# Performance work log

Hardware: AMD Instinct MI355X
Metric: run time of the kernel (lower is better)

The kernel has to match this reference:

```python
import jax, jax.numpy as jnp
import numpy as np

ROUTING_ITERS = 3
EPS = 1e-9


def squash(s):
    # s: [..., D]; faithful to the torch code: x / (1 + n^2) / sqrt(n^2 + eps)
    sq = jnp.sum(s * s, axis=-1, keepdims=True)
    return s / (1.0 + sq) / jnp.sqrt(sq + EPS)


def setup_inputs() -> dict:
    key = jax.random.key(0)
    k1, k2 = jax.random.split(key)
    B, I, C, D, d = 64, 4096, 32, 16, 16
    x = jax.random.normal(k1, (B, I, d), dtype=jnp.float32)
    weights = jax.random.normal(k2, (1, I, C, D, d), dtype=jnp.float32)
    return {"x": x, "weights": weights}


def reference(x, weights):
    # u_hat[b,i,c,D] = weights[0,i,c,D,d] @ x[b,i,d]
    u_hat = jnp.einsum('icDd,bid->bicD', weights[0], x)  # [B, I, C, D]
    B, I, C, D = u_hat.shape
    b_ij = jnp.zeros((B, I, C), dtype=u_hat.dtype)
    v_j = None
    for _ in range(ROUTING_ITERS):
        c_ij = jax.nn.softmax(b_ij, axis=2)                     # [B, I, C]
        s_j = jnp.einsum('bic,bicD->bcD', c_ij, u_hat)          # [B, C, D]
        v_j = squash(s_j)                                       # [B, C, D]
        b_ij = b_ij + jnp.einsum('bicD,bcD->bic', u_hat, v_j)   # agreement
    return v_j
```

## Files before the change

### kernel.cpp

```cpp
#include <hip/hip_runtime.h>
#include <math.h>

#define ITILES 256
#define IPB    16

typedef __bf16 bf16x8 __attribute__((ext_vector_type(8)));
typedef float  f32x16 __attribute__((ext_vector_type(16)));

__device__ inline unsigned short f2bf(float f) {
    unsigned int x = __float_as_uint(f);
    x += 0x7fff + ((x >> 16) & 1);
    return (unsigned short)(x >> 16);
}
__device__ inline float bf2f(unsigned short u) {
    return __uint_as_float(((unsigned int)u) << 16);
}
__device__ inline uint4 pack8(const unsigned short* o) {
    uint4 p;
    p.x = o[0] | ((unsigned)o[1] << 16);
    p.y = o[2] | ((unsigned)o[3] << 16);
    p.z = o[4] | ((unsigned)o[5] << 16);
    p.w = o[6] | ((unsigned)o[7] << 16);
    return p;
}

__device__ inline unsigned cvtpk(float lo, float hi) {
    unsigned r;
    asm("v_cvt_pk_bf16_f32 %0, %1, %2" : "=v"(r) : "v"(lo), "v"(hi));
    return r;
}
__device__ inline unsigned split3(float x, float y, unsigned& q2, unsigned& q3) {
    unsigned q1 = cvtpk(x, y);
    float f1x = __uint_as_float(q1 << 16);
    float f1y = __uint_as_float(q1 & 0xffff0000u);
    float rx = x - f1x, ry = y - f1y;
    q2 = cvtpk(rx, ry);
    float f2x = __uint_as_float(q2 << 16);
    float f2y = __uint_as_float(q2 & 0xffff0000u);
    q3 = cvtpk(rx - f2x, ry - f2y);
    return q1;
}

__global__ __launch_bounds__(128) void prep_x(const float* __restrict__ x,
                                              unsigned short* __restrict__ Xp)
{
    const int i = blockIdx.x;
    const int t = threadIdx.x;
    const int b = t >> 1, kh = t & 1;
    const float4* s4 = (const float4*)(x + ((size_t)b * 4096 + i) * 16 + kh * 8);
    float4 wa = s4[0], wb = s4[1];
    float wv[8] = {wa.x, wa.y, wa.z, wa.w, wb.x, wb.y, wb.z, wb.w};
    unsigned short o1[8], o2[8], o3[8];
    #pragma unroll
    for (int j = 0; j < 8; ++j) {
        float w = wv[j];
        o1[j] = f2bf(w);            float f1 = bf2f(o1[j]);
        o2[j] = f2bf(w - f1);       float f2 = bf2f(o2[j]);
        o3[j] = f2bf(w - f1 - f2);
    }
    unsigned short* dst = Xp + (size_t)i * 3072 + kh * 1536 + b * 8;
    *(uint4*)(dst)        = pack8(o1);
    *(uint4*)(dst + 512)  = pack8(o2);
    *(uint4*)(dst + 1024) = pack8(o3);
}

template<int USE_V>
__global__ __launch_bounds__(1024, 4)
void pass_kernel(const float* __restrict__ W,
                 const unsigned short* __restrict__ Xp,
                 const float* __restrict__ vg,
                 float* __restrict__ slab)
{
    __shared__ float4 vt[8192];
    __shared__ float  p_lds[32 * 65];
    __shared__ float  cij_lds[32 * 65];

    const int tid   = threadIdx.x;
    const int mt    = tid >> 6;
    const int lane  = tid & 63;
    const int l31   = lane & 31;
    const int h     = lane >> 5;
    const int cA    = 2 * mt + h;
    const int itile = blockIdx.x;
    const int i0    = itile * IPB;

    const int cW = 2 * mt + ((l31 >> 2) & 1);
    const int DW = (l31 & 3) + 4 * (l31 >> 3);
    const float4* w4 = (const float4*)(W + (size_t)i0 * 8192 + ((cW * 16 + DW) * 16 + h * 8));

    if (USE_V) {
        const float4* v4 = (const float4*)vg;
        #pragma unroll
        for (int k = 0; k < 8; ++k) {
            int idx = k * 1024 + tid;
            int b = idx >> 7, cd = idx & 127;
            vt[b * 128 + (cd ^ (b & 31))] = v4[idx];
        }
        __syncthreads();
    }

    f32x16 s0, s1;
    #pragma unroll
    for (int q = 0; q < 16; ++q) { s0[q] = 0.f; s1[q] = 0.f; }

    float4 wa = w4[0], wb = w4[1];

    #define MF(A_, B_, C_) __builtin_amdgcn_mfma_f32_32x32x16_bf16( \
        __builtin_bit_cast(bf16x8, A_), __builtin_bit_cast(bf16x8, B_), C_, 0, 0, 0)

    for (int ii = 0; ii < IPB; ++ii) {
        const int i = i0 + ii;
        const unsigned short* bb = Xp + (size_t)i * 3072 + (size_t)h * 1536 + l31 * 8;

        uint4 a1, a2, a3;
        a1.x = split3(wa.x, wa.y, a2.x, a3.x);
        a1.y = split3(wa.z, wa.w, a2.y, a3.y);
        a1.z = split3(wb.x, wb.y, a2.z, a3.z);
        a1.w = split3(wb.z, wb.w, a2.w, a3.w);

        {
            const int iin = (ii + 1 < IPB) ? (ii + 1) : ii;
            wa = w4[(size_t)iin * 2048];
            wb = w4[(size_t)iin * 2048 + 1];
        }

        if (USE_V == 0) {
            uint4 b10 = *(const uint4*)(bb);
            uint4 b11 = *(const uint4*)(bb + 256);
            uint4 b20 = *(const uint4*)(bb + 512);
            uint4 b21 = *(const uint4*)(bb + 512 + 256);
            __builtin_amdgcn_s_setprio(1);
            s0 = MF(a1, b10, s0); s1 = MF(a1, b11, s1);
            s0 = MF(a2, b10, s0); s1 = MF(a2, b11, s1);
            __builtin_amdgcn_s_setprio(0);
            uint4 b30 = *(const uint4*)(bb + 1024);
            uint4 b31 = *(const uint4*)(bb + 1024 + 256);
            __builtin_amdgcn_s_setprio(1);
            s0 = MF(a1, b20, s0); s1 = MF(a1, b21, s1);
            s0 = MF(a3, b10, s0); s1 = MF(a3, b11, s1);
            s0 = MF(a2, b20, s0); s1 = MF(a2, b21, s1);
            s0 = MF(a1, b30, s0); s1 = MF(a1, b31, s1);
            __builtin_amdgcn_s_setprio(0);
        } else {
            #pragma unroll
            for (int nt = 0; nt < 2; ++nt) {
                const unsigned short* bp = bb + nt * 256;
                uint4 b1 = *(const uint4*)(bp);
                uint4 b2 = *(const uint4*)(bp + 512);
                uint4 b3 = *(const uint4*)(bp + 1024);

                f32x16 u;
                #pragma unroll
                for (int q = 0; q < 16; ++q) u[q] = 0.f;
                __builtin_amdgcn_s_setprio(1);
                u = MF(a1, b1, u);
                u = MF(a2, b1, u);
                u = MF(a1, b2, u);
                u = MF(a3, b1, u);
                u = MF(a2, b2, u);
                u = MF(a1, b3, u);
                __builtin_amdgcn_s_setprio(0);

                const int b = nt * 32 + l31;
                float p = 0.f;
                #pragma unroll
                for (int dblk = 0; dblk < 4; ++dblk) {
                    float4 vv = vt[b * 128 + ((cA * 4 + dblk) ^ l31)];
                    p = fmaf(u[dblk * 4 + 0], vv.x, p);
                    p = fmaf(u[dblk * 4 + 1], vv.y, p);
                    p = fmaf(u[dblk * 4 + 2], vv.z, p);
                    p = fmaf(u[dblk * 4 + 3], vv.w, p);
                }
                p_lds[cA * 65 + b] = p;
                __syncthreads();

                {
                    const int bsm = nt * 32 + mt * 2 + h;
                    float e = __expf(p_lds[l31 * 65 + bsm]);
                    float t = e;
                    t += __shfl_xor(t, 16); t += __shfl_xor(t, 8);
                    t += __shfl_xor(t, 4);  t += __shfl_xor(t, 2);
                    t += __shfl_xor(t, 1);
                    cij_lds[l31 * 65 + bsm] = __fdividef(e, t);
                }
                __syncthreads();

                {
                    f32x16& ss = nt ? s1 : s0;
                    const float cij = cij_lds[cA * 65 + b];
                    #pragma unroll
                    for (int q = 0; q < 16; ++q) ss[q] = fmaf(cij, u[q], ss[q]);
                }
            }
        }
    }
    #undef MF

    float4* slab4 = (float4*)slab;
    #pragma unroll
    for (int nt = 0; nt < 2; ++nt) {
        const f32x16& ss = nt ? s1 : s0;
        const int b = nt * 32 + l31;
        size_t base = ((size_t)itile * 64 + b) * 128 + cA * 4;
        #pragma unroll
        for (int dblk = 0; dblk < 4; ++dblk) {
            float4 o = {ss[dblk * 4 + 0], ss[dblk * 4 + 1], ss[dblk * 4 + 2], ss[dblk * 4 + 3]};
            slab4[base + dblk] = o;
        }
    }
}

__global__ __launch_bounds__(256)
void reduce_squash(const float* __restrict__ slab, float* __restrict__ out, float scale,
                   const float* __restrict__ v1in, float* __restrict__ vsum)
{
    __shared__ float part[128];
    const int tid  = threadIdx.x;
    const int half = tid >> 7;
    const int o    = blockIdx.x * 128 + (tid & 127);
    float a[8];
    #pragma unroll
    for (int k = 0; k < 8; ++k) a[k] = 0.f;
    for (int g = 0; g < 16; ++g) {
        #pragma unroll
        for (int k = 0; k < 8; ++k)
            a[k] += slab[(size_t)(half * 128 + g * 8 + k) * 32768 + o];
    }
    float s = 0.f;
    #pragma unroll
    for (int k = 0; k < 8; ++k) s += a[k];
    if (half) part[tid & 127] = s;
    __syncthreads();
    if (!half) {
        s = (s + part[tid]) * scale;
        float t = s * s;
        t += __shfl_xor(t, 1);
        t += __shfl_xor(t, 2);
        t += __shfl_xor(t, 4);
        t += __shfl_xor(t, 8);
        float r = s / (1.0f + t) / sqrtf(t + 1e-9f);
        out[o] = r;
        if (v1in) vsum[o] = r + v1in[o];
    }
}

extern "C" void kernel_launch(void* const* d_in, const int* in_sizes, int n_in,
                              void* d_out, int out_size, void* d_ws, size_t ws_size,
                              hipStream_t stream)
{
    const float* x = (const float*)d_in[0];
    const float* W = (const float*)d_in[1];

    float* slab = (float*)d_ws;
    float* v1   = slab + (size_t)ITILES * 32768;
    float* v2   = v1 + 32768;
    float* v12  = v2 + 32768;
    unsigned short* Xp = (unsigned short*)(v12 + 32768);
    float* out  = (float*)d_out;

    hipLaunchKernelGGL(prep_x, dim3(4096), dim3(128), 0, stream, x, Xp);

    hipLaunchKernelGGL((pass_kernel<0>), dim3(ITILES), dim3(1024), 0, stream, W, Xp, (const float*)nullptr, slab);
    hipLaunchKernelGGL(reduce_squash,    dim3(256),    dim3(256),  0, stream, slab, v1, 1.0f / 32.0f, (const float*)nullptr, (float*)nullptr);
    hipLaunchKernelGGL((pass_kernel<1>), dim3(ITILES), dim3(1024), 0, stream, W, Xp, v1, slab);
    hipLaunchKernelGGL(reduce_squash,    dim3(256),    dim3(256),  0, stream, slab, v2, 1.0f, v1, v12);
    hipLaunchKernelGGL((pass_kernel<1>), dim3(ITILES), dim3(1024), 0, stream, W, Xp, v12, slab);
    hipLaunchKernelGGL(reduce_squash,    dim3(256),    dim3(256),  0, stream, slab, out, 1.0f, (const float*)nullptr, (float*)nullptr);
}
```

Before: 364.9 us.

## Split first routing pass into small blocks, deepen W prefetch, widen reduction grid

The first routing pass no longer needs the shared v table or barriers, so it moves to its own kernel with 256-thread blocks (four blocks per i-tile) for better scheduling and occupancy. The later passes prefetch weights two iterations ahead instead of one. The slab reduction now spreads over 1024 blocks of 32 outputs with 8 partial sums each, to use more CUs. The costs are more launched blocks and more register pressure from the deeper prefetch.

Result: slower. 375.8 us (+3.0%).

```diff
diff --git a/kernel.cpp b/kernel.cpp
--- a/kernel.cpp
+++ b/kernel.cpp
@@ -64,12 +64,85 @@
     *(uint4*)(dst + 1024) = pack8(o3);
 }
 
-template<int USE_V>
+#define MF(A_, B_, C_) __builtin_amdgcn_mfma_f32_32x32x16_bf16( \
+    __builtin_bit_cast(bf16x8, A_), __builtin_bit_cast(bf16x8, B_), C_, 0, 0, 0)
+
+__global__ __launch_bounds__(256, 5)
+void pass0_kernel(const float* __restrict__ W,
+                  const unsigned short* __restrict__ Xp,
+                  float* __restrict__ slab)
+{
+    const int tid   = threadIdx.x;
+    const int lane  = tid & 63;
+    const int l31   = lane & 31;
+    const int h     = lane >> 5;
+    const int bid   = blockIdx.x;
+    const int itile = bid >> 2;
+    const int mt    = ((bid & 3) << 2) + (tid >> 6);
+    const int cA    = 2 * mt + h;
+    const int i0    = itile * IPB;
+
+    const int cW = 2 * mt + ((l31 >> 2) & 1);
+    const int DW = (l31 & 3) + 4 * (l31 >> 3);
+    const float4* w4 = (const float4*)(W + (size_t)i0 * 8192 + ((cW * 16 + DW) * 16 + h * 8));
+
+    f32x16 s0, s1;
+    #pragma unroll
+    for (int q = 0; q < 16; ++q) { s0[q] = 0.f; s1[q] = 0.f; }
+
+    float4 wa = w4[0], wb = w4[1];
+
+    for (int ii = 0; ii < IPB; ++ii) {
+        const int i = i0 + ii;
+        const unsigned short* bb = Xp + (size_t)i * 3072 + (size_t)h * 1536 + l31 * 8;
+
+        uint4 a1, a2, a3;
+        a1.x = split3(wa.x, wa.y, a2.x, a3.x);
+        a1.y = split3(wa.z, wa.w, a2.y, a3.y);
+        a1.z = split3(wb.x, wb.y, a2.z, a3.z);
+        a1.w = split3(wb.z, wb.w, a2.w, a3.w);
+
+        {
+            const int iin = (ii + 1 < IPB) ? (ii + 1) : ii;
+            wa = w4[(size_t)iin * 2048];
+            wb = w4[(size_t)iin * 2048 + 1];
+        }
+
+        #pragma unroll
+        for (int nt = 0; nt < 2; ++nt) {
+            const unsigned short* bp = bb + nt * 256;
+            f32x16& ss = nt ? s1 : s0;
+            uint4 b1 = *(const uint4*)(bp);
+            uint4 b2 = *(const uint4*)(bp + 512);
+            ss = MF(a1, b1, ss);
+            ss = MF(a2, b1, ss);
+            uint4 b3 = *(const uint4*)(bp + 1024);
+            ss = MF(a1, b2, ss);
+            ss = MF(a3, b1, ss);
+            ss = MF(a2, b2, ss);
+            ss = MF(a1, b3, ss);
+        }
+    }
+
+    float4* slab4 = (float4*)slab;
+    #pragma unroll
+    for (int nt = 0; nt < 2; ++nt) {
+        const f32x16& ss = nt ? s1 : s0;
+        const int b = nt * 32 + l31;
+        size_t base = ((size_t)itile * 64 + b) * 128 + cA * 4;
+        #pragma unroll
+        for (int dblk = 0; dblk < 4; ++dblk) {
+            float4 o = {ss[dblk * 4 + 0], ss[dblk * 4 + 1], ss[dblk * 4 + 2], ss[dblk * 4 + 3]};
+            slab4[base + dblk] = o;
+        }
+    }
+}
+
 __global__ __launch_bounds__(1024, 4)
-void pass_kernel(const float* __restrict__ W,
-                 const unsigned short* __restrict__ Xp,
-                 const float* __restrict__ vg,
-                 float* __restrict__ slab)
+void pass1_kernel(const float* __restrict__ W,
+                  const unsigned short* __restrict__ Xp,
+                  const float* __restrict__ vg,
+                  float* __restrict__ slab)
 {
     __shared__ float4 vt[8192];
     __shared__ float  p_lds[32 * 65];
@@ -88,7 +161,7 @@
     const int DW = (l31 & 3) + 4 * (l31 >> 3);
     const float4* w4 = (const float4*)(W + (size_t)i0 * 8192 + ((cW * 16 + DW) * 16 + h * 8));
 
-    if (USE_V) {
+    {
         const float4* v4 = (const float4*)vg;
         #pragma unroll
         for (int k = 0; k < 8; ++k) {
@@ -103,98 +176,77 @@
     #pragma unroll
     for (int q = 0; q < 16; ++q) { s0[q] = 0.f; s1[q] = 0.f; }
 
-    float4 wa = w4[0], wb = w4[1];
-
-    #define MF(A_, B_, C_) __builtin_amdgcn_mfma_f32_32x32x16_bf16( \
-        __builtin_bit_cast(bf16x8, A_), __builtin_bit_cast(bf16x8, B_), C_, 0, 0, 0)
+    float4 wa0 = w4[0],    wb0 = w4[1];
+    float4 wa1 = w4[2048], wb1 = w4[2049];
 
     for (int ii = 0; ii < IPB; ++ii) {
         const int i = i0 + ii;
         const unsigned short* bb = Xp + (size_t)i * 3072 + (size_t)h * 1536 + l31 * 8;
 
         uint4 a1, a2, a3;
-        a1.x = split3(wa.x, wa.y, a2.x, a3.x);
-        a1.y = split3(wa.z, wa.w, a2.y, a3.y);
-        a1.z = split3(wb.x, wb.y, a2.z, a3.z);
-        a1.w = split3(wb.z, wb.w, a2.w, a3.w);
-
+        a1.x = split3(wa0.x, wa0.y, a2.x, a3.x);
+        a1.y = split3(wa0.z, wa0.w, a2.y, a3.y);
+        a1.z = split3(wb0.x, wb0.y, a2.z, a3.z);
+        a1.w = split3(wb0.z, wb0.w, a2.w, a3.w);
+
+        wa0 = wa1; wb0 = wb1;
         {
-            const int iin = (ii + 1 < IPB) ? (ii + 1) : ii;
-            wa = w4[(size_t)iin * 2048];
-            wb = w4[(size_t)iin * 2048 + 1];
-        }
-
-        if (USE_V == 0) {
-            uint4 b10 = *(const uint4*)(bb);
-            uint4 b11 = *(const uint4*)(bb + 256);
-            uint4 b20 = *(const uint4*)(bb + 512);
-            uint4 b21 = *(const uint4*)(bb + 512 + 256);
+            const int iin = (ii + 2 < IPB) ? (ii + 2) : (IPB - 1);
+            wa1 = w4[(size_t)iin * 2048];
+            wb1 = w4[(size_t)iin * 2048 + 1];
+        }
+
+        #pragma unroll
+        for (int nt = 0; nt < 2; ++nt) {
+            const unsigned short* bp = bb + nt * 256;
+            uint4 b1 = *(const uint4*)(bp);
+            uint4 b2 = *(const uint4*)(bp + 512);
+            uint4 b3 = *(const uint4*)(bp + 1024);
+
+            f32x16 u;
+            #pragma unroll
+            for (int q = 0; q < 16; ++q) u[q] = 0.f;
             __builtin_amdgcn_s_setprio(1);
-            s0 = MF(a1, b10, s0); s1 = MF(a1, b11, s1);
-            s0 = MF(a2, b10, s0); s1 = MF(a2, b11, s1);
+            u = MF(a1, b1, u);
+            u = MF(a2, b1, u);
+            u = MF(a1, b2, u);
+            u = MF(a3, b1, u);
+            u = MF(a2, b2, u);
+            u = MF(a1, b3, u);
             __builtin_amdgcn_s_setprio(0);
-            uint4 b30 = *(const uint4*)(bb + 1024);
-            uint4 b31 = *(const uint4*)(bb + 1024 + 256);
-            __builtin_amdgcn_s_setprio(1);
-            s0 = MF(a1, b20, s0); s1 = MF(a1, b21, s1);
-            s0 = MF(a3, b10, s0); s1 = MF(a3, b11, s1);
-            s0 = MF(a2, b20, s0); s1 = MF(a2, b21, s1);
-            s0 = MF(a1, b30, s0); s1 = MF(a1, b31, s1);
-            __builtin_amdgcn_s_setprio(0);
-        } else {
+
+            const int b = nt * 32 + l31;
+            float p = 0.f;
             #pragma unroll
-            for (int nt = 0; nt < 2; ++nt) {
-                const unsigned short* bp = bb + nt * 256;
-                uint4 b1 = *(const uint4*)(bp);
-                uint4 b2 = *(const uint4*)(bp + 512);
-                uint4 b3 = *(const uint4*)(bp + 1024);
-
-                f32x16 u;
+            for (int dblk = 0; dblk < 4; ++dblk) {
+                float4 vv = vt[b * 128 + ((cA * 4 + dblk) ^ l31)];
+                p = fmaf(u[dblk * 4 + 0], vv.x, p);
+                p = fmaf(u[dblk * 4 + 1], vv.y, p);
+                p = fmaf(u[dblk * 4 + 2], vv.z, p);
+                p = fmaf(u[dblk * 4 + 3], vv.w, p);
+            }
+            p_lds[cA * 65 + b] = p;
+            __syncthreads();
+
+            {
+                const int bsm = nt * 32 + mt * 2 + h;
+                float e = __expf(p_lds[l31 * 65 + bsm]);
+                float t = e;
+                t += __shfl_xor(t, 16); t += __shfl_xor(t, 8);
+                t += __shfl_xor(t, 4);  t += __shfl_xor(t, 2);
+                t += __shfl_xor(t, 1);
+                cij_lds[l31 * 65 + bsm] = __fdividef(e, t);
+            }
+            __syncthreads();
+
+            {
+                f32x16& ss = nt ? s1 : s0;
+                const float cij = cij_lds[cA * 65 + b];
                 #pragma unroll
-                for (int q = 0; q < 16; ++q) u[q] = 0.f;
-                __builtin_amdgcn_s_setprio(1);
-                u = MF(a1, b1, u);
-                u = MF(a2, b1, u);
-                u = MF(a1, b2, u);
-                u = MF(a3, b1, u);
-                u = MF(a2, b2, u);
-                u = MF(a1, b3, u);
-                __builtin_amdgcn_s_setprio(0);
-
-                const int b = nt * 32 + l31;
-                float p = 0.f;
-                #pragma unroll
-                for (int dblk = 0; dblk < 4; ++dblk) {
-                    float4 vv = vt[b * 128 + ((cA * 4 + dblk) ^ l31)];
-                    p = fmaf(u[dblk * 4 + 0], vv.x, p);
-                    p = fmaf(u[dblk * 4 + 1], vv.y, p);
-                    p = fmaf(u[dblk * 4 + 2], vv.z, p);
-                    p = fmaf(u[dblk * 4 + 3], vv.w, p);
-                }
-                p_lds[cA * 65 + b] = p;
-                __syncthreads();
-
-                {
-                    const int bsm = nt * 32 + mt * 2 + h;
-                    float e = __expf(p_lds[l31 * 65 + bsm]);
-                    float t = e;
-                    t += __shfl_xor(t, 16); t += __shfl_xor(t, 8);
-                    t += __shfl_xor(t, 4);  t += __shfl_xor(t, 2);
-                    t += __shfl_xor(t, 1);
-                    cij_lds[l31 * 65 + bsm] = __fdividef(e, t);
-                }
-                __syncthreads();
-
-                {
-                    f32x16& ss = nt ? s1 : s0;
-                    const float cij = cij_lds[cA * 65 + b];
-                    #pragma unroll
-                    for (int q = 0; q < 16; ++q) ss[q] = fmaf(cij, u[q], ss[q]);
-                }
+                for (int q = 0; q < 16; ++q) ss[q] = fmaf(cij, u[q], ss[q]);
             }
         }
     }
-    #undef MF
 
     float4* slab4 = (float4*)slab;
     #pragma unroll
@@ -209,30 +261,35 @@
         }
     }
 }
+#undef MF
 
 __global__ __launch_bounds__(256)
 void reduce_squash(const float* __restrict__ slab, float* __restrict__ out, float scale,
                    const float* __restrict__ v1in, float* __restrict__ vsum)
 {
-    __shared__ float part[128];
-    const int tid  = threadIdx.x;
-    const int half = tid >> 7;
-    const int o    = blockIdx.x * 128 + (tid & 127);
+    __shared__ float part[7][32];
+    const int tid = threadIdx.x;
+    const int q   = tid >> 5;
+    const int ol  = tid & 31;
+    const int o   = blockIdx.x * 32 + ol;
     float a[8];
     #pragma unroll
     for (int k = 0; k < 8; ++k) a[k] = 0.f;
-    for (int g = 0; g < 16; ++g) {
+    #pragma unroll
+    for (int g = 0; g < 4; ++g) {
         #pragma unroll
         for (int k = 0; k < 8; ++k)
-            a[k] += slab[(size_t)(half * 128 + g * 8 + k) * 32768 + o];
+            a[k] += slab[(size_t)(q * 32 + g * 8 + k) * 32768 + o];
     }
     float s = 0.f;
     #pragma unroll
     for (int k = 0; k < 8; ++k) s += a[k];
-    if (half) part[tid & 127] = s;
+    if (q) part[q - 1][ol] = s;
     __syncthreads();
-    if (!half) {
-        s = (s + part[tid]) * scale;
+    if (q == 0) {
+        #pragma unroll
+        for (int j = 0; j < 7; ++j) s += part[j][ol];
+        s *= scale;
         float t = s * s;
         t += __shfl_xor(t, 1);
         t += __shfl_xor(t, 2);
@@ -260,10 +317,10 @@
 
     hipLaunchKernelGGL(prep_x, dim3(4096), dim3(128), 0, stream, x, Xp);
 
-    hipLaunchKernelGGL((pass_kernel<0>), dim3(ITILES), dim3(1024), 0, stream, W, Xp, (const float*)nullptr, slab);
-    hipLaunchKernelGGL(reduce_squash,    dim3(256),    dim3(256),  0, stream, slab, v1, 1.0f / 32.0f, (const float*)nullptr, (float*)nullptr);
-    hipLaunchKernelGGL((pass_kernel<1>), dim3(ITILES), dim3(1024), 0, stream, W, Xp, v1, slab);
-    hipLaunchKernelGGL(reduce_squash,    dim3(256),    dim3(256),  0, stream, slab, v2, 1.0f, v1, v12);
-    hipLaunchKernelGGL((pass_kernel<1>), dim3(ITILES), dim3(1024), 0, stream, W, Xp, v12, slab);
-    hipLaunchKernelGGL(reduce_squash,    dim3(256),    dim3(256),  0, stream, slab, out, 1.0f, (const float*)nullptr, (float*)nullptr);
-}
+    hipLaunchKernelGGL(pass0_kernel,  dim3(1024), dim3(256),  0, stream, W, Xp, slab);
+    hipLaunchKernelGGL(reduce_squash, dim3(1024), dim3(256),  0, stream, slab, v1, 1.0f / 32.0f, (const float*)nullptr, (float*)nullptr);
+    hipLaunchKernelGGL(pass1_kernel,  dim3(ITILES), dim3(1024), 0, stream, W, Xp, v1, slab);
+    hipLaunchKernelGGL(reduce_squash, dim3(1024), dim3(256),  0, stream, slab, v2, 1.0f, v1, v12);
+    hipLaunchKernelGGL(pass1_kernel,  dim3(ITILES), dim3(1024), 0, stream, W, Xp, v12, slab);
+    hipLaunchKernelGGL(reduce_squash, dim3(1024), dim3(256),  0, stream, slab, out, 1.0f, (const float*)nullptr, (float*)nullptr);
+}
```
